# Kernel optimization log

Hardware: AMD Instinct MI355X
Metric: run time of the kernel (lower is better)

## Reference

```python
import jax, jax.numpy as jnp
import numpy as np
import math

D_MODEL = 1024
NUM_HEADS = 16
D_HEAD = D_MODEL // NUM_HEADS
SEQ = 2048
BATCH = 2
THETA = 10000.0
SCALE = 1.0 / math.sqrt(D_HEAD)


def rope_cos_sin(seq_len, d_head, theta):
    # freqs_cis equivalent: angles[t, j] = t * theta**(-2j/d_head)
    inv_freq = 1.0 / (theta ** (jnp.arange(0, d_head, 2, dtype=jnp.float32) / d_head))
    t = jnp.arange(seq_len, dtype=jnp.float32)
    ang = jnp.outer(t, inv_freq)  # [S, d_head//2]
    return jnp.cos(ang), jnp.sin(ang)


def apply_rope(x, cos, sin):
    # x: [B, S, H, Dh]; treat consecutive pairs as complex numbers
    B, S, H, Dh = x.shape
    xr = x.reshape(B, S, H, Dh // 2, 2)
    x0, x1 = xr[..., 0], xr[..., 1]
    c = cos[None, :, None, :]
    s = sin[None, :, None, :]
    out = jnp.stack([x0 * c - x1 * s, x0 * s + x1 * c], axis=-1)
    return out.reshape(B, S, H, Dh)


def setup_inputs() -> dict:
    key = jax.random.key(0)
    ks = jax.random.split(key, 9)
    w_std = 0.02
    return {
        "qkv": jax.random.normal(ks[0], (BATCH, SEQ, D_MODEL), jnp.float32),
        "Wq": jax.random.normal(ks[1], (D_MODEL, D_MODEL), jnp.float32) * w_std,
        "bq": jax.random.normal(ks[2], (D_MODEL,), jnp.float32) * w_std,
        "Wk": jax.random.normal(ks[3], (D_MODEL, D_MODEL), jnp.float32) * w_std,
        "bk": jax.random.normal(ks[4], (D_MODEL,), jnp.float32) * w_std,
        "Wv": jax.random.normal(ks[5], (D_MODEL, D_MODEL), jnp.float32) * w_std,
        "bv": jax.random.normal(ks[6], (D_MODEL,), jnp.float32) * w_std,
        "Wo": jax.random.normal(ks[7], (D_MODEL, D_MODEL), jnp.float32) * w_std,
        "bo": jax.random.normal(ks[8], (D_MODEL,), jnp.float32) * w_std,
    }


def reference(qkv, Wq, bq, Wk, bk, Wv, bv, Wo, bo):
    B, S, D = qkv.shape
    cos, sin = rope_cos_sin(S, D_HEAD, THETA)
    # torch Linear: y = x @ W.T + b
    q = (qkv @ Wq.T + bq).reshape(B, S, NUM_HEADS, D_HEAD)
    k = (qkv @ Wk.T + bk).reshape(B, S, NUM_HEADS, D_HEAD)
    v = (qkv @ Wv.T + bv).reshape(B, S, NUM_HEADS, D_HEAD)
    q = apply_rope(q, cos, sin)
    k = apply_rope(k, cos, sin)
    scores = jnp.einsum("bqhd,bkhd->bhqk", q, k) * SCALE
    causal = jnp.triu(jnp.ones((S, S), dtype=bool), k=1)
    scores = jnp.where(causal[None, None], -1e30, scores)
    attn = jax.nn.softmax(scores, axis=-1)
    out = jnp.einsum("bhqk,bkhd->bqhd", attn, v).reshape(B, S, D)
    return out @ Wo.T + bo
```

## Files before the change

kernel.cpp:

```cpp
#include <hip/hip_runtime.h>
#include <hip/hip_bf16.h>
#include <stdint.h>
#include <math.h>


typedef __bf16 bf16;
typedef __attribute__((ext_vector_type(4))) __bf16 bf16x4;
typedef __attribute__((ext_vector_type(8))) __bf16 bf16x8;
typedef __attribute__((ext_vector_type(4))) float f32x4;
typedef __attribute__((ext_vector_type(16))) float f32x16;
typedef __attribute__((ext_vector_type(4))) uint32_t u32x4;

#define SEQN 2048
#define DMOD 1024
#define NHEAD 16
#define DHEAD 64
#define MTOT 4096
#define VSTR 2080
#define QSCALE_LOG2E 0.18033688011112042f

__device__ __forceinline__ void gload_lds16(const bf16* g, bf16* l) {
  __builtin_amdgcn_global_load_lds(
      (const __attribute__((address_space(1))) uint32_t*)g,
      (__attribute__((address_space(3))) uint32_t*)l,
      16, 0, 0);
}

__device__ __forceinline__ uint32_t cvtpk(float lo, float hi) {
  uint32_t r;
  asm("v_cvt_pk_bf16_f32 %0, %1, %2" : "=v"(r) : "v"(lo), "v"(hi));
  return r;
}

__global__ __launch_bounds__(256) void prep_kernel(
    const float* __restrict__ X,
    const float* __restrict__ Wq, const float* __restrict__ Wk,
    const float* __restrict__ Wv, const float* __restrict__ Wo,
    bf16* __restrict__ Xb, bf16* __restrict__ Wqb, bf16* __restrict__ Wkb,
    bf16* __restrict__ Wvb, bf16* __restrict__ Wob,
    float* __restrict__ ctab, float* __restrict__ stab)
{
  const int tid = blockIdx.x * blockDim.x + threadIdx.x;
  const int nth = gridDim.x * blockDim.x;

  const float4* X4 = (const float4*)X;
  for (int i = tid; i < MTOT * DMOD / 4; i += nth) {
    float4 v = X4[i];
    bf16x4 o = { (bf16)v.x, (bf16)v.y, (bf16)v.z, (bf16)v.w };
    *(bf16x4*)(Xb + (size_t)i * 4) = o;
  }
  const float4* q4 = (const float4*)Wq;
  const float4* k4 = (const float4*)Wk;
  const float4* v4 = (const float4*)Wv;
  const float4* o4 = (const float4*)Wo;
  for (int i = tid; i < DMOD * DMOD / 4; i += nth) {
    float4 a = q4[i];
    float4 b = k4[i];
    float4 c = v4[i];
    float4 d = o4[i];
    *(bf16x4*)(Wqb + (size_t)i * 4) = bf16x4{ (bf16)a.x, (bf16)a.y, (bf16)a.z, (bf16)a.w };
    *(bf16x4*)(Wkb + (size_t)i * 4) = bf16x4{ (bf16)b.x, (bf16)b.y, (bf16)b.z, (bf16)b.w };
    *(bf16x4*)(Wvb + (size_t)i * 4) = bf16x4{ (bf16)c.x, (bf16)c.y, (bf16)c.z, (bf16)c.w };
    *(bf16x4*)(Wob + (size_t)i * 4) = bf16x4{ (bf16)d.x, (bf16)d.y, (bf16)d.z, (bf16)d.w };
  }
  for (int i = tid; i < SEQN * 32; i += nth) {
    const int s = i >> 5, p = i & 31;
    const float invf = (float)pow(10000.0, -(double)p / 32.0);
    const float ang = (float)s * invf;
    float sv, cv;
    sincosf(ang, &sv, &cv);
    ctab[i] = cv;
    stab[i] = sv;
  }
}

__global__ __launch_bounds__(256) void gemm_qkv(
    const bf16* __restrict__ Xb,
    const bf16* __restrict__ Wqb, const bf16* __restrict__ Wkb, const bf16* __restrict__ Wvb,
    const float* __restrict__ bq, const float* __restrict__ bk, const float* __restrict__ bv,
    const float* __restrict__ ctab, const float* __restrict__ stab,
    bf16* __restrict__ Qb, bf16* __restrict__ Kb, bf16* __restrict__ Vtb)
{
  __shared__ bf16 sA[3][128 * 32];
  __shared__ bf16 sB[3][128 * 32];

  const int z = blockIdx.z;
  const bf16* Bm = (z == 0) ? Wqb : (z == 1) ? Wkb : Wvb;
  const float* bias = (z == 0) ? bq : (z == 1) ? bk : bv;

  const int t = threadIdx.x;
  const int lane = t & 63, l15 = lane & 15, g = lane >> 4;
  const int wave = t >> 6, wm = wave >> 1, wn = wave & 1;
  const int tileM = blockIdx.y * 128, tileN = blockIdx.x * 128;

  f32x4 acc[4][4] = {};

  const bf16* gA = Xb + (size_t)(tileM + (t >> 2)) * DMOD + (t & 3) * 8;
  const bf16* gB = Bm + (size_t)(tileN + (t >> 2)) * DMOD + (t & 3) * 8;

  auto stage = [&](int buf, int k0) {
    gload_lds16(gA + k0, &sA[buf][t * 8]);
    gload_lds16(gA + k0 + 64 * DMOD, &sA[buf][2048 + t * 8]);
    gload_lds16(gB + k0, &sB[buf][t * 8]);
    gload_lds16(gB + k0 + 64 * DMOD, &sB[buf][2048 + t * 8]);
  };

  stage(0, 0);
  stage(1, 32);

  const int NS = DMOD / 32;
  int cur = 0;
  for (int s = 0; s < NS; ++s) {
    if (s + 2 < NS) {
      int pf = cur + 2; if (pf >= 3) pf -= 3;
      stage(pf, (s + 2) * 32);
      asm volatile("s_waitcnt vmcnt(8)" ::: "memory");
    } else if (s + 1 < NS) {
      asm volatile("s_waitcnt vmcnt(4)" ::: "memory");
    } else {
      asm volatile("s_waitcnt vmcnt(0)" ::: "memory");
    }
    __builtin_amdgcn_s_barrier();
    asm volatile("" ::: "memory");

    const bf16* cA = sA[cur];
    const bf16* cB = sB[cur];
    bf16x8 af[4], bfr[4];
#pragma unroll
    for (int i = 0; i < 4; ++i)
      af[i] = *(const bf16x8*)(cA + (wm * 64 + i * 16 + l15) * 32 + g * 8);
#pragma unroll
    for (int j = 0; j < 4; ++j)
      bfr[j] = *(const bf16x8*)(cB + (wn * 64 + j * 16 + l15) * 32 + g * 8);
#pragma unroll
    for (int i = 0; i < 4; ++i)
#pragma unroll
      for (int j = 0; j < 4; ++j)
        acc[i][j] = __builtin_amdgcn_mfma_f32_16x16x32_bf16(af[i], bfr[j], acc[i][j], 0, 0, 0);

    asm volatile("" ::: "memory");
    __builtin_amdgcn_s_barrier();
    cur = (cur == 2) ? 0 : cur + 1;
  }

#pragma unroll
  for (int j = 0; j < 4; ++j) {
    const int col = tileN + wn * 64 + j * 16 + l15;
    const float bcol = bias[col];
    const int h = col >> 6, d = col & 63;
#pragma unroll
    for (int i = 0; i < 4; ++i) {
#pragma unroll
      for (int r = 0; r < 4; ++r) {
        const int row = tileM + wm * 64 + i * 16 + g * 4 + r;
        const int b = row >> 11, s = row & (SEQN - 1);
        const float v = acc[i][j][r] + bcol;
        if (z != 2) {
          const int pair = d >> 1;
          const float cv = ctab[s * 32 + pair];
          const float sv = stab[s * 32 + pair];
          const float partner = __shfl_xor(v, 1);
          float rv = (d & 1) ? (partner * sv + v * cv) : (v * cv - partner * sv);
          if (z == 0) rv *= QSCALE_LOG2E;
          bf16* dst = (z == 0) ? Qb : Kb;
          dst[(((size_t)(b * NHEAD + h)) * SEQN + s) * DHEAD + d] = (bf16)rv;
        } else {
          Vtb[(((size_t)(b * NHEAD + h)) * DHEAD + d) * VSTR + s] = (bf16)v;
        }
      }
    }
  }
}

__global__ __launch_bounds__(256, 1) void attn_kernel(
    const bf16* __restrict__ Qb, const bf16* __restrict__ Kb,
    const bf16* __restrict__ Vt, bf16* __restrict__ AO)
{
  const int t = threadIdx.x;
  const int lane = t & 63, l31 = lane & 31, hi = lane >> 5;
  const int wave = t >> 6;

  const int bid = blockIdx.x;
  const int p = bid >> 5, bh = bid & 31;

  const bf16* Kp = Kb + (size_t)bh * SEQN * DHEAD;
  const bf16* Vp = Vt + (size_t)bh * DHEAD * VSTR;
  const bf16* Qp = Qb + (size_t)bh * SEQN * DHEAD;
  const int b = bh >> 4, h = bh & 15;

  auto prefetch = [&](bf16x8 (&K)[2][4], bf16x8 (&V)[2][4], int kv0) {
#pragma unroll
    for (int s = 0; s < 2; ++s)
#pragma unroll
      for (int ch = 0; ch < 4; ++ch)
        K[s][ch] = *(const bf16x8*)(Kp + (size_t)(kv0 + 32 * s + l31) * DHEAD + 16 * ch + 8 * hi);
#pragma unroll
    for (int dblk = 0; dblk < 2; ++dblk)
#pragma unroll
      for (int c = 0; c < 4; ++c)
        V[dblk][c] = *(const bf16x8*)(Vp + (size_t)(dblk * 32 + l31) * VSTR + kv0 + 16 * c + 8 * hi);
  };

  auto run_phase = [&](int qtile, int wrow) {
    const int qbase = qtile * 128 + wrow * 32;
    const int qg = qbase + l31;
    const int niter = (qbase >> 6) + 1;

    bf16x8 qf[4];
#pragma unroll
    for (int ch = 0; ch < 4; ++ch)
      qf[ch] = *(const bf16x8*)(Qp + (size_t)qg * DHEAD + 16 * ch + 8 * hi);

    f32x16 a0 = {}, a1 = {};
    float m = -1e30f, l = 0.f;

    auto compute = [&](const bf16x8 (&K)[2][4], const bf16x8 (&V)[2][4], int kv0) {
      f32x16 s0 = {}, s1 = {};
#pragma unroll
      for (int ch = 0; ch < 4; ++ch) {
        s0 = __builtin_amdgcn_mfma_f32_32x32x16_bf16(K[0][ch], qf[ch], s0, 0, 0, 0);
        s1 = __builtin_amdgcn_mfma_f32_32x32x16_bf16(K[1][ch], qf[ch], s1, 0, 0, 0);
      }
      float tv[32];
#pragma unroll
      for (int i = 0; i < 16; ++i) { tv[i] = s0[i]; tv[16 + i] = s1[i]; }

      if (kv0 + 63 > qbase) {
#pragma unroll
        for (int i = 0; i < 32; ++i) {
          const int key = kv0 + 32 * (i >> 4) + ((i & 3) + 8 * ((i >> 2) & 3) + 4 * hi);
          if (key > qg) tv[i] = -1e30f;
        }
      }

      float red[16];
#pragma unroll
      for (int i = 0; i < 16; ++i) red[i] = fmaxf(tv[i], tv[i + 16]);
#pragma unroll
      for (int st = 8; st >= 1; st >>= 1)
#pragma unroll
        for (int i = 0; i < st; ++i) red[i] = fmaxf(red[i], red[i + st]);
      const float tmax = fmaxf(red[0], __shfl_xor(red[0], 32));
      const float mnew = fmaxf(m, tmax);
      const float alpha = __builtin_amdgcn_exp2f(m - mnew);
      m = mnew;

#pragma unroll
      for (int i = 0; i < 32; ++i) tv[i] = __builtin_amdgcn_exp2f(tv[i] - mnew);
#pragma unroll
      for (int i = 0; i < 16; ++i) red[i] = tv[i] + tv[i + 16];
#pragma unroll
      for (int st = 8; st >= 1; st >>= 1)
#pragma unroll
        for (int i = 0; i < st; ++i) red[i] += red[i + st];
      l = l * alpha + (red[0] + __shfl_xor(red[0], 32));

#pragma unroll
      for (int i = 0; i < 16; ++i) { a0[i] *= alpha; a1[i] *= alpha; }

#pragma unroll
      for (int c = 0; c < 4; ++c) {
        const int b0 = (c & 1) * 8 + (c >> 1) * 16;
        const uint32_t P0  = cvtpk(tv[b0 + 0], tv[b0 + 1]);
        const uint32_t P0b = cvtpk(tv[b0 + 2], tv[b0 + 3]);
        const uint32_t P1  = cvtpk(tv[b0 + 4], tv[b0 + 5]);
        const uint32_t P1b = cvtpk(tv[b0 + 6], tv[b0 + 7]);
        const uint32_t sP0  = (uint32_t)__shfl_xor((int)P0, 32);
        const uint32_t sP0b = (uint32_t)__shfl_xor((int)P0b, 32);
        const uint32_t sP1  = (uint32_t)__shfl_xor((int)P1, 32);
        const uint32_t sP1b = (uint32_t)__shfl_xor((int)P1b, 32);
        u32x4 pw;
        pw[0] = hi ? sP1  : P0;
        pw[1] = hi ? sP1b : P0b;
        pw[2] = hi ? P1   : sP0;
        pw[3] = hi ? P1b  : sP0b;
        const bf16x8 pf = __builtin_bit_cast(bf16x8, pw);
        a0 = __builtin_amdgcn_mfma_f32_32x32x16_bf16(V[0][c], pf, a0, 0, 0, 0);
        a1 = __builtin_amdgcn_mfma_f32_32x32x16_bf16(V[1][c], pf, a1, 0, 0, 0);
      }
    };

    bf16x8 kA[2][4], vA[2][4], kB[2][4], vB[2][4];
    prefetch(kA, vA, 0);
    int it = 0;
    for (; it + 1 < niter; it += 2) {
      prefetch(kB, vB, (it + 1) * 64);
      compute(kA, vA, it * 64);
      if (it + 2 < niter) prefetch(kA, vA, (it + 2) * 64);
      compute(kB, vB, (it + 1) * 64);
    }
    if (it < niter) compute(kA, vA, it * 64);

    const float linv = 1.f / l;
    const size_t rowoff = ((size_t)(b * SEQN + qg)) * DMOD + h * DHEAD;
#pragma unroll
    for (int dblk = 0; dblk < 2; ++dblk) {
      const f32x16& av = dblk ? a1 : a0;
#pragma unroll
      for (int rg = 0; rg < 4; ++rg) {
        const int d0 = dblk * 32 + rg * 8 + 4 * hi;
        bf16x4 ov = { (bf16)(av[rg * 4 + 0] * linv), (bf16)(av[rg * 4 + 1] * linv),
                      (bf16)(av[rg * 4 + 2] * linv), (bf16)(av[rg * 4 + 3] * linv) };
        *(bf16x4*)(AO + rowoff + d0) = ov;
      }
    }
  };

  run_phase(p, wave);
  run_phase(15 - p, 3 - wave);
}

__global__ __launch_bounds__(256) void gemm_out(
    const bf16* __restrict__ AO, const bf16* __restrict__ Wob,
    const float* __restrict__ bo, float* __restrict__ out)
{
  __shared__ bf16 sA[3][128 * 32];
  __shared__ bf16 sB[3][128 * 32];

  const int t = threadIdx.x;
  const int lane = t & 63, l15 = lane & 15, g = lane >> 4;
  const int wave = t >> 6, wm = wave >> 1, wn = wave & 1;
  const int tileM = blockIdx.y * 128, tileN = blockIdx.x * 128;

  f32x4 acc[4][4] = {};

  const bf16* gA = AO + (size_t)(tileM + (t >> 2)) * DMOD + (t & 3) * 8;
  const bf16* gB = Wob + (size_t)(tileN + (t >> 2)) * DMOD + (t & 3) * 8;

  auto stage = [&](int buf, int k0) {
    gload_lds16(gA + k0, &sA[buf][t * 8]);
    gload_lds16(gA + k0 + 64 * DMOD, &sA[buf][2048 + t * 8]);
    gload_lds16(gB + k0, &sB[buf][t * 8]);
    gload_lds16(gB + k0 + 64 * DMOD, &sB[buf][2048 + t * 8]);
  };

  stage(0, 0);
  stage(1, 32);

  const int NS = DMOD / 32;
  int cur = 0;
  for (int s = 0; s < NS; ++s) {
    if (s + 2 < NS) {
      int pf = cur + 2; if (pf >= 3) pf -= 3;
      stage(pf, (s + 2) * 32);
      asm volatile("s_waitcnt vmcnt(8)" ::: "memory");
    } else if (s + 1 < NS) {
      asm volatile("s_waitcnt vmcnt(4)" ::: "memory");
    } else {
      asm volatile("s_waitcnt vmcnt(0)" ::: "memory");
    }
    __builtin_amdgcn_s_barrier();
    asm volatile("" ::: "memory");

    const bf16* cA = sA[cur];
    const bf16* cB = sB[cur];
    bf16x8 af[4], bfr[4];
#pragma unroll
    for (int i = 0; i < 4; ++i)
      af[i] = *(const bf16x8*)(cA + (wm * 64 + i * 16 + l15) * 32 + g * 8);
#pragma unroll
    for (int j = 0; j < 4; ++j)
      bfr[j] = *(const bf16x8*)(cB + (wn * 64 + j * 16 + l15) * 32 + g * 8);
#pragma unroll
    for (int i = 0; i < 4; ++i)
#pragma unroll
      for (int j = 0; j < 4; ++j)
        acc[i][j] = __builtin_amdgcn_mfma_f32_16x16x32_bf16(af[i], bfr[j], acc[i][j], 0, 0, 0);

    asm volatile("" ::: "memory");
    __builtin_amdgcn_s_barrier();
    cur = (cur == 2) ? 0 : cur + 1;
  }

#pragma unroll
  for (int j = 0; j < 4; ++j) {
    const int col = tileN + wn * 64 + j * 16 + l15;
    const float bcol = bo[col];
#pragma unroll
    for (int i = 0; i < 4; ++i)
#pragma unroll
      for (int r = 0; r < 4; ++r) {
        const int row = tileM + wm * 64 + i * 16 + g * 4 + r;
        out[(size_t)row * DMOD + col] = acc[i][j][r] + bcol;
      }
  }
}

extern "C" void kernel_launch(void* const* d_in, const int* in_sizes, int n_in,
                              void* d_out, int out_size, void* d_ws, size_t ws_size,
                              hipStream_t stream)
{
  (void)in_sizes; (void)n_in; (void)out_size; (void)ws_size;
  const float* X  = (const float*)d_in[0];
  const float* Wq = (const float*)d_in[1];
  const float* bq = (const float*)d_in[2];
  const float* Wk = (const float*)d_in[3];
  const float* bk = (const float*)d_in[4];
  const float* Wv = (const float*)d_in[5];
  const float* bv = (const float*)d_in[6];
  const float* Wo = (const float*)d_in[7];
  const float* bo = (const float*)d_in[8];

  char* ws = (char*)d_ws;
  float* ctab = (float*)(ws + 0);
  float* stab = (float*)(ws + 262144);
  bf16* Xb  = (bf16*)(ws + 524288);
  bf16* Wqb = (bf16*)(ws + 8912896);
  bf16* Wkb = (bf16*)(ws + 11010048);
  bf16* Wvb = (bf16*)(ws + 13107200);
  bf16* Wob = (bf16*)(ws + 15204352);
  bf16* Qb  = (bf16*)(ws + 17301504);
  bf16* Kb  = (bf16*)(ws + 25690112);
  bf16* Vtb = (bf16*)(ws + 34078720);
  bf16* AO  = (bf16*)(ws + 42598400);

  prep_kernel<<<1024, 256, 0, stream>>>(X, Wq, Wk, Wv, Wo, Xb, Wqb, Wkb, Wvb, Wob, ctab, stab);
  gemm_qkv<<<dim3(8, 32, 3), 256, 0, stream>>>(Xb, Wqb, Wkb, Wvb, bq, bk, bv, ctab, stab, Qb, Kb, Vtb);
  attn_kernel<<<256, 256, 0, stream>>>(Qb, Kb, Vtb, AO);
  gemm_out<<<dim3(8, 32), 256, 0, stream>>>(AO, Wob, bo, (float*)d_out);
}
```

Measured before the change: 142.0 us.

## Split attention KV range across wave pairs and merge partial softmax via LDS

The attention kernel moves from 256 blocks, each running two balanced query phases per wave, to 1024 blocks. Each block handles a 64-row query tile, and each pair of waves splits that tile's key/value range in half. The two partial results (accumulators, max, sum) are merged through shared memory with a flash-decoding style rescale. The launch-bounds occupancy hint is relaxed and the register double-buffered K/V prefetch is dropped in favour of a plain load-then-compute loop, which trades latency hiding for more parallelism and better load balance.

```diff
diff --git a/kernel.cpp b/kernel.cpp
--- a/kernel.cpp
+++ b/kernel.cpp
@@ -172,23 +172,34 @@
   }
 }
 
-__global__ __launch_bounds__(256, 1) void attn_kernel(
+__global__ __launch_bounds__(256) void attn_kernel(
     const bf16* __restrict__ Qb, const bf16* __restrict__ Kb,
     const bf16* __restrict__ Vt, bf16* __restrict__ AO)
 {
+  __shared__ float sMrg[2][64][35];
+
   const int t = threadIdx.x;
   const int lane = t & 63, l31 = lane & 31, hi = lane >> 5;
   const int wave = t >> 6;
+  const int sb = wave >> 1;
+  const int half = wave & 1;
 
   const int bid = blockIdx.x;
-  const int p = bid >> 5, bh = bid & 31;
+  const int bh = bid & 31;
+  const int jq = 31 - (bid >> 5);
+  const int qbase = (2 * jq + sb) * 32;
+  const int qg = qbase + l31;
+  const int n = jq + 1;
+  const int nA = (n + 1) >> 1;
+  const int kv_lo = half ? nA : 0;
+  const int kv_hi = half ? n : nA;
 
   const bf16* Kp = Kb + (size_t)bh * SEQN * DHEAD;
   const bf16* Vp = Vt + (size_t)bh * DHEAD * VSTR;
   const bf16* Qp = Qb + (size_t)bh * SEQN * DHEAD;
   const int b = bh >> 4, h = bh & 15;
 
-  auto prefetch = [&](bf16x8 (&K)[2][4], bf16x8 (&V)[2][4], int kv0) {
+  auto loadkv = [&](bf16x8 (&K)[2][4], bf16x8 (&V)[2][4], int kv0) {
 #pragma unroll
     for (int s = 0; s < 2; ++s)
 #pragma unroll
@@ -201,97 +212,103 @@
         V[dblk][c] = *(const bf16x8*)(Vp + (size_t)(dblk * 32 + l31) * VSTR + kv0 + 16 * c + 8 * hi);
   };
 
-  auto run_phase = [&](int qtile, int wrow) {
-    const int qbase = qtile * 128 + wrow * 32;
-    const int qg = qbase + l31;
-    const int niter = (qbase >> 6) + 1;
-
-    bf16x8 qf[4];
-#pragma unroll
-    for (int ch = 0; ch < 4; ++ch)
-      qf[ch] = *(const bf16x8*)(Qp + (size_t)qg * DHEAD + 16 * ch + 8 * hi);
-
-    f32x16 a0 = {}, a1 = {};
-    float m = -1e30f, l = 0.f;
-
-    auto compute = [&](const bf16x8 (&K)[2][4], const bf16x8 (&V)[2][4], int kv0) {
-      f32x16 s0 = {}, s1 = {};
-#pragma unroll
-      for (int ch = 0; ch < 4; ++ch) {
-        s0 = __builtin_amdgcn_mfma_f32_32x32x16_bf16(K[0][ch], qf[ch], s0, 0, 0, 0);
-        s1 = __builtin_amdgcn_mfma_f32_32x32x16_bf16(K[1][ch], qf[ch], s1, 0, 0, 0);
+  bf16x8 qf[4];
+#pragma unroll
+  for (int ch = 0; ch < 4; ++ch)
+    qf[ch] = *(const bf16x8*)(Qp + (size_t)qg * DHEAD + 16 * ch + 8 * hi);
+
+  f32x16 a0 = {}, a1 = {};
+  float m = -1e30f, l = 0.f;
+
+  auto compute = [&](const bf16x8 (&K)[2][4], const bf16x8 (&V)[2][4], int kv0) {
+    f32x16 s0 = {}, s1 = {};
+#pragma unroll
+    for (int ch = 0; ch < 4; ++ch) {
+      s0 = __builtin_amdgcn_mfma_f32_32x32x16_bf16(K[0][ch], qf[ch], s0, 0, 0, 0);
+      s1 = __builtin_amdgcn_mfma_f32_32x32x16_bf16(K[1][ch], qf[ch], s1, 0, 0, 0);
+    }
+    float tv[32];
+#pragma unroll
+    for (int i = 0; i < 16; ++i) { tv[i] = s0[i]; tv[16 + i] = s1[i]; }
+
+    if (kv0 + 63 > qbase) {
+#pragma unroll
+      for (int i = 0; i < 32; ++i) {
+        const int key = kv0 + 32 * (i >> 4) + ((i & 3) + 8 * ((i >> 2) & 3) + 4 * hi);
+        if (key > qg) tv[i] = -1e30f;
       }
-      float tv[32];
-#pragma unroll
-      for (int i = 0; i < 16; ++i) { tv[i] = s0[i]; tv[16 + i] = s1[i]; }
-
-      if (kv0 + 63 > qbase) {
-#pragma unroll
-        for (int i = 0; i < 32; ++i) {
-          const int key = kv0 + 32 * (i >> 4) + ((i & 3) + 8 * ((i >> 2) & 3) + 4 * hi);
-          if (key > qg) tv[i] = -1e30f;
-        }
-      }
-
-      float red[16];
-#pragma unroll
-      for (int i = 0; i < 16; ++i) red[i] = fmaxf(tv[i], tv[i + 16]);
-#pragma unroll
-      for (int st = 8; st >= 1; st >>= 1)
-#pragma unroll
-        for (int i = 0; i < st; ++i) red[i] = fmaxf(red[i], red[i + st]);
-      const float tmax = fmaxf(red[0], __shfl_xor(red[0], 32));
-      const float mnew = fmaxf(m, tmax);
-      const float alpha = __builtin_amdgcn_exp2f(m - mnew);
-      m = mnew;
-
-#pragma unroll
-      for (int i = 0; i < 32; ++i) tv[i] = __builtin_amdgcn_exp2f(tv[i] - mnew);
-#pragma unroll
-      for (int i = 0; i < 16; ++i) red[i] = tv[i] + tv[i + 16];
-#pragma unroll
-      for (int st = 8; st >= 1; st >>= 1)
-#pragma unroll
-        for (int i = 0; i < st; ++i) red[i] += red[i + st];
-      l = l * alpha + (red[0] + __shfl_xor(red[0], 32));
-
-#pragma unroll
-      for (int i = 0; i < 16; ++i) { a0[i] *= alpha; a1[i] *= alpha; }
-
-#pragma unroll
-      for (int c = 0; c < 4; ++c) {
-        const int b0 = (c & 1) * 8 + (c >> 1) * 16;
-        const uint32_t P0  = cvtpk(tv[b0 + 0], tv[b0 + 1]);
-        const uint32_t P0b = cvtpk(tv[b0 + 2], tv[b0 + 3]);
-        const uint32_t P1  = cvtpk(tv[b0 + 4], tv[b0 + 5]);
-        const uint32_t P1b = cvtpk(tv[b0 + 6], tv[b0 + 7]);
-        const uint32_t sP0  = (uint32_t)__shfl_xor((int)P0, 32);
-        const uint32_t sP0b = (uint32_t)__shfl_xor((int)P0b, 32);
-        const uint32_t sP1  = (uint32_t)__shfl_xor((int)P1, 32);
-        const uint32_t sP1b = (uint32_t)__shfl_xor((int)P1b, 32);
-        u32x4 pw;
-        pw[0] = hi ? sP1  : P0;
-        pw[1] = hi ? sP1b : P0b;
-        pw[2] = hi ? P1   : sP0;
-        pw[3] = hi ? P1b  : sP0b;
-        const bf16x8 pf = __builtin_bit_cast(bf16x8, pw);
-        a0 = __builtin_amdgcn_mfma_f32_32x32x16_bf16(V[0][c], pf, a0, 0, 0, 0);
-        a1 = __builtin_amdgcn_mfma_f32_32x32x16_bf16(V[1][c], pf, a1, 0, 0, 0);
-      }
-    };
-
-    bf16x8 kA[2][4], vA[2][4], kB[2][4], vB[2][4];
-    prefetch(kA, vA, 0);
-    int it = 0;
-    for (; it + 1 < niter; it += 2) {
-      prefetch(kB, vB, (it + 1) * 64);
-      compute(kA, vA, it * 64);
-      if (it + 2 < niter) prefetch(kA, vA, (it + 2) * 64);
-      compute(kB, vB, (it + 1) * 64);
-    }
-    if (it < niter) compute(kA, vA, it * 64);
-
-    const float linv = 1.f / l;
+    }
+
+    float red[16];
+#pragma unroll
+    for (int i = 0; i < 16; ++i) red[i] = fmaxf(tv[i], tv[i + 16]);
+#pragma unroll
+    for (int st = 8; st >= 1; st >>= 1)
+#pragma unroll
+      for (int i = 0; i < st; ++i) red[i] = fmaxf(red[i], red[i + st]);
+    const float tmax = fmaxf(red[0], __shfl_xor(red[0], 32));
+    const float mnew = fmaxf(m, tmax);
+    const float alpha = __builtin_amdgcn_exp2f(m - mnew);
+    m = mnew;
+
+#pragma unroll
+    for (int i = 0; i < 32; ++i) tv[i] = __builtin_amdgcn_exp2f(tv[i] - mnew);
+#pragma unroll
+    for (int i = 0; i < 16; ++i) red[i] = tv[i] + tv[i + 16];
+#pragma unroll
+    for (int st = 8; st >= 1; st >>= 1)
+#pragma unroll
+      for (int i = 0; i < st; ++i) red[i] += red[i + st];
+    l = l * alpha + (red[0] + __shfl_xor(red[0], 32));
+
+#pragma unroll
+    for (int i = 0; i < 16; ++i) { a0[i] *= alpha; a1[i] *= alpha; }
+
+#pragma unroll
+    for (int c = 0; c < 4; ++c) {
+      const int b0 = (c & 1) * 8 + (c >> 1) * 16;
+      const uint32_t P0  = cvtpk(tv[b0 + 0], tv[b0 + 1]);
+      const uint32_t P0b = cvtpk(tv[b0 + 2], tv[b0 + 3]);
+      const uint32_t P1  = cvtpk(tv[b0 + 4], tv[b0 + 5]);
+      const uint32_t P1b = cvtpk(tv[b0 + 6], tv[b0 + 7]);
+      const uint32_t sP0  = (uint32_t)__shfl_xor((int)P0, 32);
+      const uint32_t sP0b = (uint32_t)__shfl_xor((int)P0b, 32);
+      const uint32_t sP1  = (uint32_t)__shfl_xor((int)P1, 32);
+      const uint32_t sP1b = (uint32_t)__shfl_xor((int)P1b, 32);
+      u32x4 pw;
+      pw[0] = hi ? sP1  : P0;
+      pw[1] = hi ? sP1b : P0b;
+      pw[2] = hi ? P1   : sP0;
+      pw[3] = hi ? P1b  : sP0b;
+      const bf16x8 pf = __builtin_bit_cast(bf16x8, pw);
+      a0 = __builtin_amdgcn_mfma_f32_32x32x16_bf16(V[0][c], pf, a0, 0, 0, 0);
+      a1 = __builtin_amdgcn_mfma_f32_32x32x16_bf16(V[1][c], pf, a1, 0, 0, 0);
+    }
+  };
+
+  for (int it = kv_lo; it < kv_hi; ++it) {
+    bf16x8 K[2][4], V[2][4];
+    loadkv(K, V, it * 64);
+    compute(K, V, it * 64);
+  }
+
+  if (half) {
+#pragma unroll
+    for (int i = 0; i < 16; ++i) {
+      sMrg[sb][lane][i] = a0[i];
+      sMrg[sb][lane][16 + i] = a1[i];
+    }
+    sMrg[sb][lane][32] = m;
+    sMrg[sb][lane][33] = l;
+  }
+  __syncthreads();
+  if (!half) {
+    const float mB = sMrg[sb][lane][32];
+    const float lB = sMrg[sb][lane][33];
+    const float ms = fmaxf(m, mB);
+    const float fA = __builtin_amdgcn_exp2f(m - ms);
+    const float fB = __builtin_amdgcn_exp2f(mB - ms);
+    const float linv = 1.f / (l * fA + lB * fB);
     const size_t rowoff = ((size_t)(b * SEQN + qg)) * DMOD + h * DHEAD;
 #pragma unroll
     for (int dblk = 0; dblk < 2; ++dblk) {
@@ -299,15 +316,14 @@
 #pragma unroll
       for (int rg = 0; rg < 4; ++rg) {
         const int d0 = dblk * 32 + rg * 8 + 4 * hi;
-        bf16x4 ov = { (bf16)(av[rg * 4 + 0] * linv), (bf16)(av[rg * 4 + 1] * linv),
-                      (bf16)(av[rg * 4 + 2] * linv), (bf16)(av[rg * 4 + 3] * linv) };
+        bf16x4 ov;
+#pragma unroll
+        for (int e = 0; e < 4; ++e)
+          ov[e] = (bf16)((av[rg * 4 + e] * fA + sMrg[sb][lane][dblk * 16 + rg * 4 + e] * fB) * linv);
         *(bf16x4*)(AO + rowoff + d0) = ov;
       }
     }
-  };
-
-  run_phase(p, wave);
-  run_phase(15 - p, 3 - wave);
+  }
 }
 
 __global__ __launch_bounds__(256) void gemm_out(
@@ -416,6 +432,6 @@
 
   prep_kernel<<<1024, 256, 0, stream>>>(X, Wq, Wk, Wv, Wo, Xb, Wqb, Wkb, Wvb, Wob, ctab, stab);
   gemm_qkv<<<dim3(8, 32, 3), 256, 0, stream>>>(Xb, Wqb, Wkb, Wvb, bq, bk, bv, ctab, stab, Qb, Kb, Vtb);
-  attn_kernel<<<256, 256, 0, stream>>>(Qb, Kb, Vtb, AO);
+  attn_kernel<<<1024, 256, 0, stream>>>(Qb, Kb, Vtb, AO);
   gemm_out<<<dim3(8, 32), 256, 0, stream>>>(AO, Wob, bo, (float*)d_out);
 }
```

Measured after the change: 147.1 us. +3.6%, slower.
